# Optimization experiments

Hardware: AMD Instinct MI355X
Metric: run time of the kernel (lower is better)

Reference implementation:

```python
import jax, jax.numpy as jnp
import numpy as np

EPS = 1e-5
K = 3          # lisa kernel taps
GROUP = 4      # lisa groups
DILS = (3, 5, 7)


def ln4d(x, g, b):
    # LayerNormalization4D: stats over channel dim; torch uses sqrt(clamp(var, eps))
    mu = x.mean(axis=1, keepdims=True)
    var = ((x - mu) ** 2).mean(axis=1, keepdims=True)
    std = jnp.sqrt(jnp.maximum(var, EPS))
    return (x - mu) / std * g[None, :, None, None] + b[None, :, None, None]


def ln4dcf(x, g, b):
    # LayerNormalization4DCF: stats over (C, F) dims of [B,C,T,F]; sqrt(var + eps)
    mu = x.mean(axis=(1, 3), keepdims=True)
    var = ((x - mu) ** 2).mean(axis=(1, 3), keepdims=True)
    return (x - mu) / jnp.sqrt(var + EPS) * g[None, :, None, :] + b[None, :, None, :]


def prelu(x, a):
    return jnp.where(x >= 0, x, a * x)


def lisa(x, conv_w, inside_all, lamb_l, lamb_h, dilation, horizontal):
    # unfold-based local gated conv-attention
    n, c, h, w = x.shape
    pad = dilation  # = dilation * (K - 1) // 2 for K == 3
    # global avg pool -> 1x1 conv -> tanh: per-(group, tap) scalar filter
    filt = jnp.tanh(x.mean(axis=(2, 3)) @ conv_w.T).reshape(n, GROUP, K)
    # expand group weights to per-channel (channel cc belongs to group cc // (c//GROUP))
    wc = jnp.repeat(filt, c // GROUP, axis=1)  # [n, c, K]
    axis = 3 if horizontal else 2
    padw = [(0, 0)] * 4
    padw[axis] = (pad, pad)
    xp = jnp.pad(x, padw, mode='reflect')  # ReflectionPad2d
    L = w if horizontal else h
    out = jnp.zeros_like(x)
    for ki in range(K):  # fixed 3 taps: shifted-slice form of F.unfold
        sl = jax.lax.slice_in_dim(xp, ki * dilation, ki * dilation + L, axis=axis)
        out = out + sl * wc[:, :, ki][:, :, None, None]
    gap = x.mean(axis=axis, keepdims=True)  # AdaptiveAvgPool2d((None,1)) / ((1,None))
    ia = inside_all[None, :, None, None]
    out_low = (out * (ia + 1.0) - ia * gap) * lamb_l[None, :, None, None]
    return out_low + x * (lamb_h[None, :, None, None] + 1.0)


def forward(x, br_g, br_b, lisa_w, lisa_in, lisa_ll, lisa_lh, mix_gamma, mix_beta,
            convb_w, convb_b, gn_g, gn_b, convb_a,
            q_w, q_b, q_a, q_lng, q_lnb,
            k_w, k_b, k_a, k_lng, k_lnb,
            v_w, v_b, v_a, v_lng, v_lnb,
            proj_w, proj_b, proj_a, proj_lng, proj_lnb):
    B, C, T, F = x.shape
    bsum = jnp.zeros_like(x)
    for i in range(3):  # three dilation branches, each: intra (freq axis) then inter (time axis)
        b = lisa(ln4d(x, br_g[i], br_b[i]), lisa_w[i], lisa_in[i], lisa_ll[i], lisa_lh[i], DILS[i], True)
        b = lisa(ln4d(b, br_g[i + 3], br_b[i + 3]), lisa_w[i + 3], lisa_in[i + 3], lisa_ll[i + 3], lisa_lh[i + 3], DILS[i], False)
        bsum = bsum + mix_gamma[i][None, :, None, None] * b + x * mix_beta[i][None, :, None, None]
    # conv_b: 1x1 conv -> GroupNorm(1, C) -> PReLU
    y = jnp.einsum('bctf,oc->botf', bsum, convb_w) + convb_b[None, :, None, None]
    mu = y.mean(axis=(1, 2, 3), keepdims=True)
    var = ((y - mu) ** 2).mean(axis=(1, 2, 3), keepdims=True)
    y = (y - mu) / jnp.sqrt(var + EPS) * gn_g[None, :, None, None] + gn_b[None, :, None, None]
    output = prelu(y, convb_a)

    def head_proj(wt, bs, a, lng, lnb):
        # per-head 1x1 conv -> PReLU -> LN4DCF, vectorized over heads
        z = jnp.einsum('bctf,hec->hbetf', output, wt) + bs[:, None, :, None, None]
        z = prelu(z, a[:, None, None, None, None])
        mz = z.mean(axis=(2, 4), keepdims=True)
        vz = ((z - mz) ** 2).mean(axis=(2, 4), keepdims=True)
        return (z - mz) / jnp.sqrt(vz + EPS) * lng[:, None, :, None, :] + lnb[:, None, :, None, :]

    Q = head_proj(q_w, q_b, q_a, q_lng, q_lnb)   # [H,B,E,T,F]
    Kh = head_proj(k_w, k_b, k_a, k_lng, k_lnb)  # [H,B,E,T,F]
    V = head_proj(v_w, v_b, v_a, v_lng, v_lnb)   # [H,B,D,T,F]
    H, E, D = q_w.shape[0], q_w.shape[1], v_w.shape[1]
    Qm = Q.transpose(0, 1, 3, 2, 4).reshape(H, B, T, E * F)
    Km = Kh.transpose(0, 1, 3, 2, 4).reshape(H, B, T, E * F)
    Vm = V.transpose(0, 1, 3, 2, 4).reshape(H, B, T, D * F)
    scale = float(np.sqrt(E * F))
    attn = jax.nn.softmax(jnp.einsum('hbtd,hbsd->hbts', Qm, Km) / scale, axis=-1)
    o = jnp.einsum('hbts,hbsd->hbtd', attn, Vm).reshape(H, B, T, D, F)
    o = o.transpose(1, 0, 3, 2, 4).reshape(B, H * D, T, F)  # matches torch view/transpose chain
    o = prelu(jnp.einsum('bctf,oc->botf', o, proj_w) + proj_b[None, :, None, None], proj_a)
    o = ln4dcf(o, proj_lng, proj_lnb)
    return o + output


def setup_inputs():
    B, C, T, F = 4, 64, 1000, 129
    H, E, D = 4, 4, 16  # E = ceil(512/129), D = C // H
    ks = iter(jax.random.split(jax.random.key(0), 64))
    r = lambda shape, s=0.1: jax.random.normal(next(ks), shape, dtype=jnp.float32) * s
    return dict(
        x=jax.random.normal(next(ks), (B, C, T, F), dtype=jnp.float32),
        br_g=1.0 + r((6, C)), br_b=r((6, C)),
        lisa_w=r((6, GROUP * K, C)), lisa_in=r((6, C)), lisa_ll=r((6, C)), lisa_lh=r((6, C)),
        mix_gamma=r((3, C)), mix_beta=1.0 + r((3, C)),
        convb_w=r((C, C)), convb_b=r((C,)), gn_g=1.0 + r((C,)), gn_b=r((C,)),
        convb_a=jnp.asarray(0.25, jnp.float32),
        q_w=r((H, E, C)), q_b=r((H, E)), q_a=0.25 + r((H,)), q_lng=1.0 + r((H, E, F)), q_lnb=r((H, E, F)),
        k_w=r((H, E, C)), k_b=r((H, E)), k_a=0.25 + r((H,)), k_lng=1.0 + r((H, E, F)), k_lnb=r((H, E, F)),
        v_w=r((H, D, C)), v_b=r((H, D)), v_a=0.25 + r((H,)), v_lng=1.0 + r((H, D, F)), v_lnb=r((H, D, F)),
        proj_w=r((C, C)), proj_b=r((C,)), proj_a=jnp.asarray(0.25, jnp.float32),
        proj_lng=1.0 + r((C, F)), proj_lnb=r((C, F)),
    )


def reference(x, br_g, br_b, lisa_w, lisa_in, lisa_ll, lisa_lh, mix_gamma, mix_beta,
              convb_w, convb_b, gn_g, gn_b, convb_a,
              q_w, q_b, q_a, q_lng, q_lnb,
              k_w, k_b, k_a, k_lng, k_lnb,
              v_w, v_b, v_a, v_lng, v_lnb,
              proj_w, proj_b, proj_a, proj_lng, proj_lnb):
    return forward(x, br_g, br_b, lisa_w, lisa_in, lisa_ll, lisa_lh, mix_gamma, mix_beta,
                   convb_w, convb_b, gn_g, gn_b, convb_a,
                   q_w, q_b, q_a, q_lng, q_lnb,
                   k_w, k_b, k_a, k_lng, k_lnb,
                   v_w, v_b, v_a, v_lng, v_lnb,
                   proj_w, proj_b, proj_a, proj_lng, proj_lnb)
```

## Files before the change

kernel.cpp:

```cpp
#include <hip/hip_runtime.h>
#include <hip/hip_bf16.h>

#define Bz 4
#define Cc 64
#define Tt 1000
#define Ff 129
#define TF 129000
#define CTF 8256000
#define SZ 33024000L
#define EPSv 1e-5f

#define KQK 544
#define KPV 1024
#define LDP 2000
#define NV 2064

typedef __attribute__((ext_vector_type(8))) short bf16x8;
typedef __attribute__((ext_vector_type(4))) float f32x4;

__device__ __forceinline__ ushort bf_bits(__hip_bfloat16 h){
  union { __hip_bfloat16 h; ushort u; } c; c.h = h; return c.u;
}
__device__ __forceinline__ float bits_f32(ushort u){
  union { float f; unsigned int i; } c; c.i = ((unsigned int)u) << 16; return c.f;
}

__device__ __forceinline__ float wave_sum(float v){
#pragma unroll
  for (int o = 32; o; o >>= 1) v += __shfl_down(v, o, 64);
  return v;
}
__device__ __forceinline__ float wave_bcast_sum(float v){
#pragma unroll
  for (int o = 1; o < 64; o <<= 1) v += __shfl_xor(v, o, 64);
  return v;
}
__device__ __forceinline__ float blk_sum256(float v, float* red){
  __syncthreads();
  v = wave_sum(v);
  int tid = threadIdx.x;
  if ((tid & 63) == 0) red[tid >> 6] = v;
  __syncthreads();
  return red[0] + red[1] + red[2] + red[3];
}
__device__ __forceinline__ float blk_max256(float v, float* red){
  __syncthreads();
#pragma unroll
  for (int o = 32; o; o >>= 1) v = fmaxf(v, __shfl_down(v, o, 64));
  int tid = threadIdx.x;
  if ((tid & 63) == 0) red[tid >> 6] = v;
  __syncthreads();
  return fmaxf(fmaxf(red[0], red[1]), fmaxf(red[2], red[3]));
}

__global__ void k_zero8(float* s){ if (threadIdx.x < 8) s[threadIdx.x] = 0.f; }
__global__ void k_zerop(float* ps){
  int i = blockIdx.x*256 + threadIdx.x;
  if (i < 8000) ps[i] = 0.f;
}

__global__ __launch_bounds__(256) void k_ln4d(const float* __restrict__ in, float* __restrict__ out,
                       const float* __restrict__ g, const float* __restrict__ be){
  int gid = blockIdx.x*256 + threadIdx.x;
  if (gid >= Bz*TF) return;
  int b = gid / TF, p = gid - b*TF;
  size_t base = (size_t)b*CTF + p;
  float v[64]; float s1 = 0.f, s2 = 0.f;
#pragma unroll
  for (int c = 0; c < 64; c++){ float x = in[base + (size_t)c*TF]; v[c] = x; s1 += x; s2 += x*x; }
  float mu = s1*(1.f/64.f);
  float var = s2*(1.f/64.f) - mu*mu;
  float rstd = rsqrtf(fmaxf(var, EPSv));
#pragma unroll
  for (int c = 0; c < 64; c++) out[base + (size_t)c*TF] = (v[c]-mu)*rstd*g[c] + be[c];
}

__global__ void k_chmean(const float* __restrict__ in, float* __restrict__ m){
  int bc = blockIdx.x;
  const float4* p = (const float4*)(in + (size_t)bc*TF);
  float s = 0.f;
  for (int i = threadIdx.x; i < TF/4; i += 256){ float4 u = p[i]; s += u.x+u.y+u.z+u.w; }
  __shared__ float red[4];
  s = blk_sum256(s, red);
  if (threadIdx.x == 0) m[bc] = s * (1.f/(float)TF);
}

__global__ void k_filt(const float* __restrict__ m, const float* __restrict__ w, float* __restrict__ filt){
  int t = threadIdx.x;
  if (t >= Bz*12) return;
  int b = t/12, gk = t - b*12;
  float s = 0.f;
  for (int c = 0; c < 64; c++) s += m[b*64+c]*w[gk*64+c];
  filt[t] = tanhf(s);
}

__global__ void k_lisa_h(const float* __restrict__ in, float* __restrict__ out,
                         const float* __restrict__ filt, const float* __restrict__ iap,
                         const float* __restrict__ llp, const float* __restrict__ lhp, int dil){
  __shared__ float r[132];
  int row = blockIdx.x;
  int c = (row / Tt) % Cc;
  int b = row / (Tt*Cc);
  size_t base = (size_t)row * Ff;
  int lane = threadIdx.x;
  float s = 0.f;
  for (int f = lane; f < Ff; f += 64){ float x = in[base+f]; r[f] = x; s += x; }
  s = wave_bcast_sum(s);
  float gap = s * (1.f/129.f);
  __syncthreads();
  int g3 = b*12 + (c>>4)*3;
  float w0 = filt[g3], w1 = filt[g3+1], w2 = filt[g3+2];
  float ia = iap[c], ll = llp[c], lh1 = lhp[c] + 1.f, ia1 = ia + 1.f;
  for (int f = lane; f < Ff; f += 64){
    int fm = f - dil; fm = fm < 0 ? -fm : fm;
    int fp = f + dil; fp = fp > 128 ? 256 - fp : fp;
    float conv = w0*r[fm] + w1*r[f] + w2*r[fp];
    out[base+f] = (conv*ia1 - ia*gap)*ll + r[f]*lh1;
  }
}

__global__ void k_colmean(const float* __restrict__ in, float* __restrict__ gapv){
  int lane = threadIdx.x & 63, strip = threadIdx.x >> 6;
  int f = blockIdx.x*64 + lane;
  int c = blockIdx.y, b = blockIdx.z;
  size_t cb = ((size_t)(b*Cc + c))*TF + f;
  float s = 0.f;
  if (f < Ff){ for (int t = strip; t < Tt; t += 4) s += in[cb + (size_t)t*Ff]; }
  __shared__ float sm[256];
  sm[threadIdx.x] = s; __syncthreads();
  if (strip == 0 && f < Ff){
    float tot = sm[threadIdx.x] + sm[threadIdx.x+64] + sm[threadIdx.x+128] + sm[threadIdx.x+192];
    gapv[(b*Cc + c)*Ff + f] = tot * (1.f/(float)Tt);
  }
}

__global__ void k_lisa_v(const float* __restrict__ in, const float* __restrict__ x,
                         float* __restrict__ A, const float* __restrict__ filt,
                         const float* __restrict__ gapv,
                         const float* __restrict__ iap, const float* __restrict__ llp,
                         const float* __restrict__ lhp,
                         const float* __restrict__ mgp, const float* __restrict__ mbp,
                         int dil, int accum){
  int lane = threadIdx.x & 63, strip = threadIdx.x >> 6;
  int ftile = blockIdx.x % 3, tch = blockIdx.x / 3;
  int f = ftile*64 + lane;
  if (f >= Ff) return;
  int c = blockIdx.y, b = blockIdx.z;
  int g3 = b*12 + (c>>4)*3;
  float w0 = filt[g3], w1 = filt[g3+1], w2 = filt[g3+2];
  float ia = iap[c], ll = llp[c], lh1 = lhp[c]+1.f, ia1 = ia+1.f;
  float mg = mgp[c], mb = mbp[c];
  float gap = gapv[(b*Cc+c)*Ff + f];
  size_t cb = ((size_t)(b*Cc + c))*TF + f;
  int tend = tch*100 + 100;
  for (int t = tch*100 + strip; t < tend; t += 4){
    int tm = t - dil; tm = tm < 0 ? -tm : tm;
    int tp = t + dil; tp = tp > 999 ? 1998 - tp : tp;
    float vm = in[cb + (size_t)tm*Ff];
    float vc = in[cb + (size_t)t*Ff];
    float vp = in[cb + (size_t)tp*Ff];
    float conv = w0*vm + w1*vc + w2*vp;
    float val = (conv*ia1 - ia*gap)*ll + vc*lh1;
    float o = mg*val + mb*x[cb + (size_t)t*Ff];
    size_t oi = cb + (size_t)t*Ff;
    A[oi] = accum ? (A[oi] + o) : o;
  }
}

__global__ __launch_bounds__(256) void k_convb(const float* __restrict__ in, float* __restrict__ out,
                        const float* __restrict__ W, const float* __restrict__ bias,
                        float* __restrict__ stat){
  __shared__ float bacc[8];
  if (threadIdx.x < 8) bacc[threadIdx.x] = 0.f;
  __syncthreads();
  int gid = blockIdx.x*256 + threadIdx.x;
  float s1 = 0.f, s2 = 0.f;
  int b = 0;
  if (gid < Bz*TF){
    b = gid / TF;
    int p = gid - b*TF;
    size_t base = (size_t)b*CTF + p;
    float v[64];
#pragma unroll
    for (int c = 0; c < 64; c++) v[c] = in[base + (size_t)c*TF];
    for (int o = 0; o < 64; o++){
      float s = bias[o];
      const float4* w4 = (const float4*)&W[o*64];
#pragma unroll
      for (int c = 0; c < 16; c++){
        float4 w = w4[c];
        s += v[4*c]*w.x + v[4*c+1]*w.y + v[4*c+2]*w.z + v[4*c+3]*w.w;
      }
      out[base + (size_t)o*TF] = s;
      s1 += s; s2 += s*s;
    }
  }
  int blo = __shfl(b, 0, 64), bhi = __shfl(b, 63, 64);
  if (blo == bhi){
    float w1 = wave_sum(s1), w2 = wave_sum(s2);
    if ((threadIdx.x & 63) == 0){ atomicAdd(&bacc[blo*2], w1); atomicAdd(&bacc[blo*2+1], w2); }
  } else {
    atomicAdd(&bacc[b*2], s1); atomicAdd(&bacc[b*2+1], s2);
  }
  __syncthreads();
  if (threadIdx.x < 8 && bacc[threadIdx.x] != 0.f) atomicAdd(&stat[threadIdx.x], bacc[threadIdx.x]);
}

__global__ void k_gnapply(float* __restrict__ y, const float* __restrict__ g,
                          const float* __restrict__ be, const float* __restrict__ a,
                          const float* __restrict__ stat){
  size_t gid = (size_t)blockIdx.x*256 + threadIdx.x;
  if (gid >= (size_t)(SZ/4)) return;
  size_t e0 = gid*4;
  int b = (int)(e0 / CTF);
  int c = (int)((e0 / TF) & 63);
  float mu = stat[b*2] * (1.f/(float)CTF);
  float var = stat[b*2+1] * (1.f/(float)CTF) - mu*mu;
  float rstd = rsqrtf(var + EPSv);
  float gc = g[c], bc = be[c], al = a[0];
  float4 v = *(const float4*)(y + e0);
  float o[4] = {v.x, v.y, v.z, v.w};
#pragma unroll
  for (int i = 0; i < 4; i++){
    float z = (o[i]-mu)*rstd*gc + bc;
    o[i] = z >= 0.f ? z : al*z;
  }
  *(float4*)(y + e0) = make_float4(o[0], o[1], o[2], o[3]);
}

__global__ __launch_bounds__(256) void k_qkvP(const float* __restrict__ Y,
    const float* __restrict__ qw, const float* __restrict__ qb, const float* __restrict__ qa,
    const float* __restrict__ kw, const float* __restrict__ kb, const float* __restrict__ ka,
    const float* __restrict__ vw, const float* __restrict__ vb, const float* __restrict__ va,
    __hip_bfloat16* __restrict__ Z){
  __shared__ float Ws[96*64];
  __shared__ float Bs[96], As[96];
  for (int i = threadIdx.x; i < 96*64; i += 256){
    int r = i >> 6, c = i & 63;
    float w;
    if (r < 16) w = qw[(r)*64 + c];
    else if (r < 32) w = kw[(r-16)*64 + c];
    else w = vw[(r-32)*64 + c];
    Ws[i] = w;
  }
  if (threadIdx.x < 96){
    int r = threadIdx.x;
    if (r < 16){ Bs[r] = qb[r]; As[r] = qa[r>>2]; }
    else if (r < 32){ Bs[r] = kb[r-16]; As[r] = ka[(r-16)>>2]; }
    else { Bs[r] = vb[r-32]; As[r] = va[(r-32)>>4]; }
  }
  __syncthreads();
  int gid = blockIdx.x*256 + threadIdx.x;
  if (gid >= Bz*TF) return;
  int b = gid / TF, p = gid - b*TF;
  size_t base = (size_t)b*CTF + p;
  float v[64];
#pragma unroll
  for (int c = 0; c < 64; c++) v[c] = Y[base + (size_t)c*TF];
  __hip_bfloat16* zb = Z + ((size_t)b*96)*TF + p;
  for (int r = 0; r < 96; r++){
    float s = Bs[r];
    const float4* w4 = (const float4*)&Ws[r*64];
#pragma unroll
    for (int c = 0; c < 16; c++){
      float4 w = w4[c];
      s += v[4*c]*w.x + v[4*c+1]*w.y + v[4*c+2]*w.z + v[4*c+3]*w.w;
    }
    s = s >= 0.f ? s : As[r]*s;
    zb[(size_t)r*TF] = __float2bfloat16(s);
  }
}

__global__ __launch_bounds__(256) void k_qkvN(const __hip_bfloat16* __restrict__ Z,
    const float* __restrict__ qg, const float* __restrict__ qz,
    const float* __restrict__ kg, const float* __restrict__ kz,
    const float* __restrict__ vg, const float* __restrict__ vz,
    __hip_bfloat16* __restrict__ Qm, __hip_bfloat16* __restrict__ Km,
    __hip_bfloat16* __restrict__ Vm){
  __shared__ ushort zt[96*129];
  __shared__ float ps1[256], ps2[256];
  __shared__ float mug[12], rsg[12];
  int t = blockIdx.x, b = blockIdx.y;
  const ushort* Zb = (const ushort*)(Z + ((size_t)b*96)*TF + (size_t)t*Ff);
  int tid = threadIdx.x;
  int u = tid/10, l = tid - u*10;
  int kind = 0, h = 0, jbase = 0, g = 0, rbase = 0;
  bool act = tid < 240;
  if (act){
    if (u < 4){ kind = 0; h = u; jbase = 0; g = h; rbase = h*4; }
    else if (u < 8){ kind = 1; h = u-4; jbase = 0; g = 4+h; rbase = 16+h*4; }
    else { int uv = u-8; kind = 2; h = uv>>2; jbase = (uv&3)*516; g = 8+h; rbase = 32+h*16; }
  }
  float s1 = 0.f, s2 = 0.f;
  if (act){
    for (int j = jbase + l; j < jbase + 516; j += 10){
      int e = j/129, f = j - e*129;
      int r = rbase + e;
      ushort raw = Zb[(size_t)r*TF + f];
      float z = bits_f32(raw);
      s1 += z; s2 += z*z;
      zt[r*129 + f] = raw;
    }
  }
  ps1[tid] = s1; ps2[tid] = s2;
  __syncthreads();
  if (tid < 12){
    int t0, cnt; float n;
    if (tid < 8){ t0 = tid*10; cnt = 10; n = 516.f; }
    else { t0 = (8 + (tid-8)*4)*10; cnt = 40; n = 2064.f; }
    float a = 0.f, q = 0.f;
    for (int i = 0; i < cnt; i++){ a += ps1[t0+i]; q += ps2[t0+i]; }
    float mu = a/n;
    mug[tid] = mu;
    rsg[tid] = rsqrtf(q/n - mu*mu + EPSv);
  }
  __syncthreads();
  if (act){
    float mu = mug[g], rs = rsg[g];
    size_t obase = (size_t)(h*Bz + b)*Tt + t;
    const float* lg; const float* lb; __hip_bfloat16* outp;
    if (kind == 0){ lg = qg + h*516; lb = qz + h*516; outp = Qm + obase*KQK; }
    else if (kind == 1){ lg = kg + h*516; lb = kz + h*516; outp = Km + obase*KQK; }
    else { lg = vg + h*2064; lb = vz + h*2064; outp = Vm + obase*NV; }
    for (int j = jbase + l; j < jbase + 516; j += 10){
      int e = j/129, f = j - e*129;
      int r = rbase + e;
      float z = bits_f32(zt[r*129 + f]);
      float val = (z - mu)*rs*lg[j] + lb[j];
      outp[j] = __float2bfloat16(val);
    }
  } else {
    int i0 = (tid - 240)*14;
    for (int i = i0; i < i0 + 14; i++){
      int kk = i/112, pj = i - kk*112;
      int hh = pj/28, off = 516 + (pj - hh*28);
      size_t obase = (size_t)(hh*Bz + b)*Tt + t;
      (kk ? Km : Qm)[obase*KQK + off] = __float2bfloat16(0.f);
    }
  }
}

__global__ void k_vt(const ushort* __restrict__ Vm, ushort* __restrict__ Vt){
  __shared__ ushort tile[64][72];
  int t0 = blockIdx.x*64, n0 = blockIdx.y*64, hb = blockIdx.z;
  const ushort* src = Vm + (size_t)hb*Tt*NV;
  ushort* dst = Vt + (size_t)hb*NV*KPV;
  int nl = threadIdx.x & 63, tl = threadIdx.x >> 6;
#pragma unroll
  for (int i = 0; i < 16; i++){
    int t = tl + i*4;
    int gt = t0 + t, gn = n0 + nl;
    ushort v = 0;
    if (gt < Tt && gn < NV) v = src[(size_t)gt*NV + gn];
    tile[t][nl] = v;
  }
  __syncthreads();
  int tl2 = threadIdx.x & 63, nl2 = threadIdx.x >> 6;
#pragma unroll
  for (int i = 0; i < 16; i++){
    int n = nl2 + i*4;
    int gn = n0 + n;
    if (gn < NV) dst[(size_t)gn*KPV + t0 + tl2] = tile[tl2][n];
  }
}

template<int MODE>
__global__ __launch_bounds__(256) void k_gemm(
    const ushort* __restrict__ A, int lda, long strideA,
    const ushort* __restrict__ Bt, int ldb, long strideB,
    float* __restrict__ C, long strideC,
    int M, int N, int Kc, float alpha){
  __shared__ ushort As[128*40];
  __shared__ ushort Bs[128*40];
  int hb = blockIdx.z;
  const ushort* Ab = A + (long)hb*strideA;
  const ushort* Bb = Bt + (long)hb*strideB;
  int i0 = blockIdx.y*128, j0 = blockIdx.x*128;
  int tid = threadIdx.x;
  int wave = tid >> 6, lane = tid & 63;
  int wm = (wave >> 1)*64, wn = (wave & 1)*64;
  int col16 = lane & 15, quad = lane >> 4;
  f32x4 acc[4][4] = {};
  int srow = tid >> 2;
  int scol = (tid & 3)*8;
  for (int k0 = 0; k0 < Kc; k0 += 32){
#pragma unroll
    for (int r = 0; r < 2; r++){
      int row = srow + r*64;
      int gi = i0 + row;
      float4 va = (gi < M) ? *(const float4*)(Ab + (long)gi*lda + k0 + scol)
                           : make_float4(0.f,0.f,0.f,0.f);
      *(float4*)&As[row*40 + scol] = va;
      int gj = j0 + row;
      float4 vb = (gj < N) ? *(const float4*)(Bb + (long)gj*ldb + k0 + scol)
                           : make_float4(0.f,0.f,0.f,0.f);
      *(float4*)&Bs[row*40 + scol] = vb;
    }
    __syncthreads();
    bf16x8 af[4], bfr[4];
#pragma unroll
    for (int mt = 0; mt < 4; mt++) af[mt]  = *(const bf16x8*)&As[(wm + mt*16 + col16)*40 + quad*8];
#pragma unroll
    for (int nt = 0; nt < 4; nt++) bfr[nt] = *(const bf16x8*)&Bs[(wn + nt*16 + col16)*40 + quad*8];
#pragma unroll
    for (int mt = 0; mt < 4; mt++)
#pragma unroll
      for (int nt = 0; nt < 4; nt++)
        acc[mt][nt] = __builtin_amdgcn_mfma_f32_16x16x32_bf16(af[mt], bfr[nt], acc[mt][nt], 0, 0, 0);
    __syncthreads();
  }
  if (MODE == 0){
    float* Cb = C + (long)hb*strideC;
#pragma unroll
    for (int mt = 0; mt < 4; mt++){
      int ibase = i0 + wm + mt*16 + quad*4;
#pragma unroll
      for (int nt = 0; nt < 4; nt++){
        int j = j0 + wn + nt*16 + col16;
        if (j < N){
#pragma unroll
          for (int rg = 0; rg < 4; rg++){
            int i = ibase + rg;
            if (i < M) Cb[(long)i*N + j] = acc[mt][nt][rg]*alpha;
          }
        }
      }
    }
  } else {
    int h = hb >> 2, b = hb & 3;
#pragma unroll
    for (int mt = 0; mt < 4; mt++){
      int ibase = i0 + wm + mt*16 + quad*4;
#pragma unroll
      for (int nt = 0; nt < 4; nt++){
        int n = j0 + wn + nt*16 + col16;
        if (n < NV){
          int d = n / 129, f = n - d*129;
          float* oc = C + ((long)(b*64 + h*16 + d)*Tt)*Ff + f;
#pragma unroll
          for (int rg = 0; rg < 4; rg++){
            int i = ibase + rg;
            if (i < M) oc[(long)i*Ff] = acc[mt][nt][rg];
          }
        }
      }
    }
  }
}

__global__ void k_softmax(float* __restrict__ S){
  float* row = S + (size_t)blockIdx.x * Tt;
  __hip_bfloat16* prow = (__hip_bfloat16*)row;
  int tid = threadIdx.x;
  __shared__ float red[4];
  float lv[4];
#pragma unroll
  for (int k = 0; k < 4; k++){ int idx = tid + k*256; lv[k] = (idx < Tt) ? row[idx] : -1e30f; }
  float m = fmaxf(fmaxf(lv[0], lv[1]), fmaxf(lv[2], lv[3]));
  m = blk_max256(m, red);
  float s = 0.f;
#pragma unroll
  for (int k = 0; k < 4; k++){ lv[k] = __expf(lv[k]-m); s += lv[k]; }
  s = blk_sum256(s, red);
  float inv = 1.f/s;
#pragma unroll
  for (int k = 0; k < 4; k++){
    int idx = tid + k*256;
    prow[idx] = __float2bfloat16(idx < Tt ? lv[k]*inv : 0.f);
  }
}

__global__ __launch_bounds__(256) void k_projA(const float* __restrict__ in, float* __restrict__ out,
    const float* __restrict__ W, const float* __restrict__ bias,
    const float* __restrict__ pa, float* __restrict__ pstat){
  int gid = blockIdx.x*256 + threadIdx.x;
  float s1 = 0.f, s2 = 0.f;
  int r = 3999;
  if (gid < Bz*TF){
    int b = gid / TF;
    int p = gid - b*TF;
    r = gid / 129;
    size_t base = (size_t)b*CTF + p;
    float al = pa[0];
    float v[64];
#pragma unroll
    for (int c = 0; c < 64; c++) v[c] = in[base + (size_t)c*TF];
    for (int o = 0; o < 64; o++){
      float s = bias[o];
      const float4* w4 = (const float4*)&W[o*64];
#pragma unroll
      for (int c = 0; c < 16; c++){
        float4 w = w4[c];
        s += v[4*c]*w.x + v[4*c+1]*w.y + v[4*c+2]*w.z + v[4*c+3]*w.w;
      }
      s = s >= 0.f ? s : al*s;
      out[base + (size_t)o*TF] = s;
      s1 += s; s2 += s*s;
    }
  }
  int rlo = __shfl(r, 0, 64), rhi = __shfl(r, 63, 64);
  if (rlo == rhi){
    float a1 = wave_sum(s1), a2 = wave_sum(s2);
    if ((threadIdx.x & 63) == 0){
      atomicAdd(&pstat[rlo*2], a1); atomicAdd(&pstat[rlo*2+1], a2);
    }
  } else {
    bool lo = (r == rlo);
    float a1 = wave_sum(lo ? s1 : 0.f);
    float a2 = wave_sum(lo ? s2 : 0.f);
    float b1 = wave_sum(lo ? 0.f : s1);
    float b2 = wave_sum(lo ? 0.f : s2);
    if ((threadIdx.x & 63) == 0){
      atomicAdd(&pstat[rlo*2], a1); atomicAdd(&pstat[rlo*2+1], a2);
      atomicAdd(&pstat[rhi*2], b1); atomicAdd(&pstat[rhi*2+1], b2);
    }
  }
}

__global__ __launch_bounds__(256) void k_projB(const float* __restrict__ proj,
    const float* __restrict__ Y, float* __restrict__ Out,
    const float* __restrict__ pstat, const float* __restrict__ lng,
    const float* __restrict__ lnb){
  int t = blockIdx.x, b = blockIdx.y;
  int r = b*1000 + t;
  const float n = 64.f*129.f;
  float mu = pstat[r*2] / n;
  float var = pstat[r*2+1] / n - mu*mu;
  float rstd = rsqrtf(var + EPSv);
  size_t base = (size_t)b*CTF + (size_t)t*Ff;
  for (int idx = threadIdx.x; idx < 64*Ff; idx += 256){
    int c = idx / Ff, f = idx - c*Ff;
    size_t off = base + (size_t)c*TF + f;
    Out[off] = (proj[off]-mu)*rstd*lng[idx] + lnb[idx] + Y[off];
  }
}

extern "C" void kernel_launch(void* const* d_in, const int* in_sizes, int n_in,
                              void* d_out, int out_size, void* d_ws, size_t ws_size,
                              hipStream_t stream){
  const float* x       = (const float*)d_in[0];
  const float* br_g    = (const float*)d_in[1];
  const float* br_b    = (const float*)d_in[2];
  const float* lisa_w  = (const float*)d_in[3];
  const float* lisa_in = (const float*)d_in[4];
  const float* lisa_ll = (const float*)d_in[5];
  const float* lisa_lh = (const float*)d_in[6];
  const float* mix_g   = (const float*)d_in[7];
  const float* mix_b   = (const float*)d_in[8];
  const float* convb_w = (const float*)d_in[9];
  const float* convb_b = (const float*)d_in[10];
  const float* gn_g    = (const float*)d_in[11];
  const float* gn_b    = (const float*)d_in[12];
  const float* convb_a = (const float*)d_in[13];
  const float* q_w  = (const float*)d_in[14];
  const float* q_b  = (const float*)d_in[15];
  const float* q_a  = (const float*)d_in[16];
  const float* q_lg = (const float*)d_in[17];
  const float* q_lb = (const float*)d_in[18];
  const float* k_w  = (const float*)d_in[19];
  const float* k_b  = (const float*)d_in[20];
  const float* k_a  = (const float*)d_in[21];
  const float* k_lg = (const float*)d_in[22];
  const float* k_lb = (const float*)d_in[23];
  const float* v_w  = (const float*)d_in[24];
  const float* v_b  = (const float*)d_in[25];
  const float* v_a  = (const float*)d_in[26];
  const float* v_lg = (const float*)d_in[27];
  const float* v_lb = (const float*)d_in[28];
  const float* p_w  = (const float*)d_in[29];
  const float* p_b  = (const float*)d_in[30];
  const float* p_a  = (const float*)d_in[31];
  const float* p_lg = (const float*)d_in[32];
  const float* p_lb = (const float*)d_in[33];

  float* out  = (float*)d_out;
  float* buf0 = (float*)d_ws;
  float* buf1 = buf0 + SZ;
  float* buf2 = buf1 + SZ;
  float* chm  = buf2 + SZ;
  float* filt = chm + 256;
  float* stat = filt + 64;
  float* gapv = stat + 16;
  float* pstat = gapv;

  if (ws_size < (3*(size_t)SZ + 40000)*sizeof(float)) return;

  __hip_bfloat16* Qm = (__hip_bfloat16*)buf2;
  __hip_bfloat16* Km = Qm + (size_t)16*Tt*KQK;
  __hip_bfloat16* Vm = Km + (size_t)16*Tt*KQK;
  __hip_bfloat16* Z  = (__hip_bfloat16*)buf0;
  ushort* Vt = (ushort*)buf0;
  float*  S  = buf0 + (size_t)16*NV*KPV/2;

  k_zero8<<<1, 64, 0, stream>>>(stat);

  const int dils[3] = {3, 5, 7};
  for (int i = 0; i < 3; i++){
    k_ln4d<<<2016, 256, 0, stream>>>(x, buf1, br_g + i*64, br_b + i*64);
    k_chmean<<<256, 256, 0, stream>>>(buf1, chm);
    k_filt<<<1, 64, 0, stream>>>(chm, lisa_w + i*768, filt);
    k_lisa_h<<<Bz*Cc*Tt, 64, 0, stream>>>(buf1, buf2, filt, lisa_in + i*64, lisa_ll + i*64, lisa_lh + i*64, dils[i]);
    k_ln4d<<<2016, 256, 0, stream>>>(buf2, buf1, br_g + (i+3)*64, br_b + (i+3)*64);
    k_chmean<<<256, 256, 0, stream>>>(buf1, chm);
    k_filt<<<1, 64, 0, stream>>>(chm, lisa_w + (i+3)*768, filt);
    k_colmean<<<dim3(3, 64, 4), 256, 0, stream>>>(buf1, gapv);
    k_lisa_v<<<dim3(30, 64, 4), 256, 0, stream>>>(buf1, x, buf0, filt, gapv,
        lisa_in + (i+3)*64, lisa_ll + (i+3)*64, lisa_lh + (i+3)*64,
        mix_g + i*64, mix_b + i*64, dils[i], i > 0 ? 1 : 0);
  }
  k_convb<<<2016, 256, 0, stream>>>(buf0, buf1, convb_w, convb_b, stat);
  k_gnapply<<<32250, 256, 0, stream>>>(buf1, gn_g, gn_b, convb_a, stat);
  k_qkvP<<<2016, 256, 0, stream>>>(buf1, q_w, q_b, q_a, k_w, k_b, k_a, v_w, v_b, v_a, Z);
  k_qkvN<<<dim3(1000, 4), 256, 0, stream>>>(Z, q_lg, q_lb, k_lg, k_lb, v_lg, v_lb, Qm, Km, Vm);
  k_vt<<<dim3(16, 33, 16), 256, 0, stream>>>((const ushort*)Vm, Vt);
  k_gemm<0><<<dim3(8, 8, 16), 256, 0, stream>>>(
      (const ushort*)Qm, KQK, (long)Tt*KQK,
      (const ushort*)Km, KQK, (long)Tt*KQK,
      S, (long)Tt*Tt, Tt, Tt, KQK, 0.04402254531f);
  k_softmax<<<16000, 256, 0, stream>>>(S);
  k_gemm<1><<<dim3(17, 8, 16), 256, 0, stream>>>(
      (const ushort*)S, LDP, (long)Tt*LDP,
      Vt, KPV, (long)NV*KPV,
      out, 0, Tt, NV, KPV, 1.f);
  k_zerop<<<32, 256, 0, stream>>>(pstat);
  k_projA<<<2016, 256, 0, stream>>>(out, buf0, p_w, p_b, p_a, pstat);
  k_projB<<<dim3(1000, 4), 256, 0, stream>>>(buf0, buf1, out, pstat, p_lg, p_lb);
}
```

Baseline: 2.830 ms.

## Fuse channel-mean reduction into LayerNorm kernel via atomics; drop qkvP shared weights

The per-(batch,channel) mean is now accumulated inside k_ln4d. Each wave sums its normalized values and adds them atomically into a zero-initialized buffer, with a separate slot per LISA stage. This removes six full-tensor k_chmean read passes, at the cost of atomic traffic and float summation-order nondeterminism. Separately, k_qkvP stops staging weights in shared memory and reads them straight from global memory (uniform loads), which removes the LDS fill and barrier but may raise load latency.

```diff
diff --git a/kernel.cpp b/kernel.cpp
--- a/kernel.cpp
+++ b/kernel.cpp
@@ -53,36 +53,54 @@
   return fmaxf(fmaxf(red[0], red[1]), fmaxf(red[2], red[3]));
 }
 
-__global__ void k_zero8(float* s){ if (threadIdx.x < 8) s[threadIdx.x] = 0.f; }
+__global__ void k_zeroinit(float* stat, float* chm){
+  int i = blockIdx.x*256 + threadIdx.x;
+  if (i < 8) stat[i] = 0.f;
+  if (i < 1536) chm[i] = 0.f;
+}
 __global__ void k_zerop(float* ps){
   int i = blockIdx.x*256 + threadIdx.x;
   if (i < 8000) ps[i] = 0.f;
 }
 
 __global__ __launch_bounds__(256) void k_ln4d(const float* __restrict__ in, float* __restrict__ out,
-                       const float* __restrict__ g, const float* __restrict__ be){
+                       const float* __restrict__ g, const float* __restrict__ be,
+                       float* __restrict__ chm){
   int gid = blockIdx.x*256 + threadIdx.x;
-  if (gid >= Bz*TF) return;
-  int b = gid / TF, p = gid - b*TF;
-  size_t base = (size_t)b*CTF + p;
-  float v[64]; float s1 = 0.f, s2 = 0.f;
-#pragma unroll
-  for (int c = 0; c < 64; c++){ float x = in[base + (size_t)c*TF]; v[c] = x; s1 += x; s2 += x*x; }
-  float mu = s1*(1.f/64.f);
-  float var = s2*(1.f/64.f) - mu*mu;
-  float rstd = rsqrtf(fmaxf(var, EPSv));
-#pragma unroll
-  for (int c = 0; c < 64; c++) out[base + (size_t)c*TF] = (v[c]-mu)*rstd*g[c] + be[c];
-}
-
-__global__ void k_chmean(const float* __restrict__ in, float* __restrict__ m){
-  int bc = blockIdx.x;
-  const float4* p = (const float4*)(in + (size_t)bc*TF);
-  float s = 0.f;
-  for (int i = threadIdx.x; i < TF/4; i += 256){ float4 u = p[i]; s += u.x+u.y+u.z+u.w; }
-  __shared__ float red[4];
-  s = blk_sum256(s, red);
-  if (threadIdx.x == 0) m[bc] = s * (1.f/(float)TF);
+  bool valid = gid < Bz*TF;
+  int b = 0;
+  float v[64];
+  if (valid){
+    b = gid / TF;
+    int p = gid - b*TF;
+    size_t base = (size_t)b*CTF + p;
+    float s1 = 0.f, s2 = 0.f;
+#pragma unroll
+    for (int c = 0; c < 64; c++){ float x = in[base + (size_t)c*TF]; v[c] = x; s1 += x; s2 += x*x; }
+    float mu = s1*(1.f/64.f);
+    float var = s2*(1.f/64.f) - mu*mu;
+    float rstd = rsqrtf(fmaxf(var, EPSv));
+#pragma unroll
+    for (int c = 0; c < 64; c++){
+      float o = (v[c]-mu)*rstd*g[c] + be[c];
+      v[c] = o;
+      out[base + (size_t)c*TF] = o;
+    }
+  } else {
+#pragma unroll
+    for (int c = 0; c < 64; c++) v[c] = 0.f;
+  }
+  unsigned long long bal = __ballot(valid);
+  int blo = __shfl(b, 0, 64), bhi = __shfl(b, 63, 64);
+  if (bal == ~0ull && blo == bhi){
+#pragma unroll
+    for (int c = 0; c < 64; c++){
+      float s = wave_sum(v[c]);
+      if ((threadIdx.x & 63) == 0) atomicAdd(&chm[blo*64 + c], s);
+    }
+  } else if (valid){
+    for (int c = 0; c < 64; c++) atomicAdd(&chm[b*64 + c], v[c]);
+  }
 }
 
 __global__ void k_filt(const float* __restrict__ m, const float* __restrict__ w, float* __restrict__ filt){
@@ -91,7 +109,7 @@
   int b = t/12, gk = t - b*12;
   float s = 0.f;
   for (int c = 0; c < 64; c++) s += m[b*64+c]*w[gk*64+c];
-  filt[t] = tanhf(s);
+  filt[t] = tanhf(s * (1.f/(float)TF));
 }
 
 __global__ void k_lisa_h(const float* __restrict__ in, float* __restrict__ out,
@@ -233,23 +251,6 @@
     const float* __restrict__ kw, const float* __restrict__ kb, const float* __restrict__ ka,
     const float* __restrict__ vw, const float* __restrict__ vb, const float* __restrict__ va,
     __hip_bfloat16* __restrict__ Z){
-  __shared__ float Ws[96*64];
-  __shared__ float Bs[96], As[96];
-  for (int i = threadIdx.x; i < 96*64; i += 256){
-    int r = i >> 6, c = i & 63;
-    float w;
-    if (r < 16) w = qw[(r)*64 + c];
-    else if (r < 32) w = kw[(r-16)*64 + c];
-    else w = vw[(r-32)*64 + c];
-    Ws[i] = w;
-  }
-  if (threadIdx.x < 96){
-    int r = threadIdx.x;
-    if (r < 16){ Bs[r] = qb[r]; As[r] = qa[r>>2]; }
-    else if (r < 32){ Bs[r] = kb[r-16]; As[r] = ka[(r-16)>>2]; }
-    else { Bs[r] = vb[r-32]; As[r] = va[(r-32)>>4]; }
-  }
-  __syncthreads();
   int gid = blockIdx.x*256 + threadIdx.x;
   if (gid >= Bz*TF) return;
   int b = gid / TF, p = gid - b*TF;
@@ -258,16 +259,41 @@
 #pragma unroll
   for (int c = 0; c < 64; c++) v[c] = Y[base + (size_t)c*TF];
   __hip_bfloat16* zb = Z + ((size_t)b*96)*TF + p;
-  for (int r = 0; r < 96; r++){
-    float s = Bs[r];
-    const float4* w4 = (const float4*)&Ws[r*64];
+  for (int r = 0; r < 16; r++){
+    float s = qb[r];
+    const float4* w4 = (const float4*)&qw[r*64];
 #pragma unroll
     for (int c = 0; c < 16; c++){
       float4 w = w4[c];
       s += v[4*c]*w.x + v[4*c+1]*w.y + v[4*c+2]*w.z + v[4*c+3]*w.w;
     }
-    s = s >= 0.f ? s : As[r]*s;
+    float al = qa[r>>2];
+    s = s >= 0.f ? s : al*s;
     zb[(size_t)r*TF] = __float2bfloat16(s);
+  }
+  for (int r = 0; r < 16; r++){
+    float s = kb[r];
+    const float4* w4 = (const float4*)&kw[r*64];
+#pragma unroll
+    for (int c = 0; c < 16; c++){
+      float4 w = w4[c];
+      s += v[4*c]*w.x + v[4*c+1]*w.y + v[4*c+2]*w.z + v[4*c+3]*w.w;
+    }
+    float al = ka[r>>2];
+    s = s >= 0.f ? s : al*s;
+    zb[(size_t)(16+r)*TF] = __float2bfloat16(s);
+  }
+  for (int r = 0; r < 64; r++){
+    float s = vb[r];
+    const float4* w4 = (const float4*)&vw[r*64];
+#pragma unroll
+    for (int c = 0; c < 16; c++){
+      float4 w = w4[c];
+      s += v[4*c]*w.x + v[4*c+1]*w.y + v[4*c+2]*w.z + v[4*c+3]*w.w;
+    }
+    float al = va[r>>4];
+    s = s >= 0.f ? s : al*s;
+    zb[(size_t)(32+r)*TF] = __float2bfloat16(s);
   }
 }
 
@@ -578,7 +604,7 @@
   float* buf1 = buf0 + SZ;
   float* buf2 = buf1 + SZ;
   float* chm  = buf2 + SZ;
-  float* filt = chm + 256;
+  float* filt = chm + 1536;
   float* stat = filt + 64;
   float* gapv = stat + 16;
   float* pstat = gapv;
@@ -592,17 +618,15 @@
   ushort* Vt = (ushort*)buf0;
   float*  S  = buf0 + (size_t)16*NV*KPV/2;
 
-  k_zero8<<<1, 64, 0, stream>>>(stat);
+  k_zeroinit<<<8, 256, 0, stream>>>(stat, chm);
 
   const int dils[3] = {3, 5, 7};
   for (int i = 0; i < 3; i++){
-    k_ln4d<<<2016, 256, 0, stream>>>(x, buf1, br_g + i*64, br_b + i*64);
-    k_chmean<<<256, 256, 0, stream>>>(buf1, chm);
-    k_filt<<<1, 64, 0, stream>>>(chm, lisa_w + i*768, filt);
+    k_ln4d<<<2016, 256, 0, stream>>>(x, buf1, br_g + i*64, br_b + i*64, chm + i*256);
+    k_filt<<<1, 64, 0, stream>>>(chm + i*256, lisa_w + i*768, filt);
     k_lisa_h<<<Bz*Cc*Tt, 64, 0, stream>>>(buf1, buf2, filt, lisa_in + i*64, lisa_ll + i*64, lisa_lh + i*64, dils[i]);
-    k_ln4d<<<2016, 256, 0, stream>>>(buf2, buf1, br_g + (i+3)*64, br_b + (i+3)*64);
-    k_chmean<<<256, 256, 0, stream>>>(buf1, chm);
-    k_filt<<<1, 64, 0, stream>>>(chm, lisa_w + (i+3)*768, filt);
+    k_ln4d<<<2016, 256, 0, stream>>>(buf2, buf1, br_g + (i+3)*64, br_b + (i+3)*64, chm + (3+i)*256);
+    k_filt<<<1, 64, 0, stream>>>(chm + (3+i)*256, lisa_w + (i+3)*768, filt);
     k_colmean<<<dim3(3, 64, 4), 256, 0, stream>>>(buf1, gapv);
     k_lisa_v<<<dim3(30, 64, 4), 256, 0, stream>>>(buf1, x, buf0, filt, gapv,
         lisa_in + (i+3)*64, lisa_ll + (i+3)*64, lisa_lh + (i+3)*64,
```

After: 11.01 ms. 289% more time.
